# Kernel tuning notes

Measured on AMD Instinct MI355X. Metric: run time of the kernel, lower is better.

The kernel has to match this reference:

```python
import jax, jax.numpy as jnp
import numpy as np

H = 1024
S = 32768

def setup_inputs() -> dict:
    key = jax.random.key(0)
    k1, k2, k3, k4 = jax.random.split(key, 4)
    hidden = jax.random.normal(k1, (H,), dtype=jnp.float32)
    encoder_outputs = jax.random.normal(k2, (S, H), dtype=jnp.float32)
    # nn.Linear(H, H) params, scaled like torch default init
    bound = 1.0 / np.sqrt(H)
    W = jax.random.uniform(k3, (H, H), minval=-bound, maxval=bound, dtype=jnp.float32)
    b = jax.random.uniform(k4, (H,), minval=-bound, maxval=bound, dtype=jnp.float32)
    return {"hidden": hidden, "encoder_outputs": encoder_outputs, "W": W, "b": b}

def reference(hidden, encoder_outputs, W, b):
    # method == 'general': energy_i = hidden . (W @ e_i + b)
    # batched over all timesteps in one matmul instead of a Python loop
    proj = jnp.einsum('sh,dh->sd', encoder_outputs, W) + b  # [S, H]
    energies = proj @ hidden                                 # [S]
    attn = jax.nn.softmax(energies)                          # softmax over seq_len
    return attn[None, None, :]                               # [1, 1, S]
```

## Files before the change

### kernel.cpp

```cpp
#include <hip/hip_runtime.h>
#include <math.h>

#define H 1024
#define S 32768


__global__ __launch_bounds__(256) void compute_v(const float* __restrict__ W,
                                                 const float* __restrict__ hidden,
                                                 float* __restrict__ v) {
    int h = blockIdx.x * 256 + threadIdx.x;
    int d0 = blockIdx.y * 16;
    float acc = 0.f;
#pragma unroll
    for (int j = 0; j < 16; ++j) {
        int d = d0 + j;
        acc += W[(size_t)d * H + h] * hidden[d];
    }
    atomicAdd(&v[h], acc);
}

__global__ __launch_bounds__(256) void energies_kernel(const float* __restrict__ enc,
                                                       const float* __restrict__ v,
                                                       float* __restrict__ energies,
                                                       float* __restrict__ pmax,
                                                       float* __restrict__ psum) {
    const int lane = threadIdx.x & 63;
    const int wave = threadIdx.x >> 6;

    const float4* v4 = (const float4*)v;
    float4 va = v4[lane];
    float4 vb = v4[64 + lane];
    float4 vc = v4[128 + lane];
    float4 vd = v4[192 + lane];

    float m = -INFINITY;
    float sum = 0.f;

    int s0 = blockIdx.x * 32 + wave * 8;
#pragma unroll 1
    for (int r = 0; r < 8; ++r) {
        int s = s0 + r;
        const float4* row = (const float4*)(enc + (size_t)s * H);
        float4 a = row[lane];
        float4 b = row[64 + lane];
        float4 c = row[128 + lane];
        float4 d = row[192 + lane];
        float dot = a.x * va.x + a.y * va.y + a.z * va.z + a.w * va.w;
        dot += b.x * vb.x + b.y * vb.y + b.z * vb.z + b.w * vb.w;
        dot += c.x * vc.x + c.y * vc.y + c.z * vc.z + c.w * vc.w;
        dot += d.x * vd.x + d.y * vd.y + d.z * vd.z + d.w * vd.w;
#pragma unroll
        for (int off = 32; off > 0; off >>= 1) dot += __shfl_xor(dot, off, 64);
        if (lane == 0) energies[s] = dot;
        float mnew = fmaxf(m, dot);
        sum = sum * __expf(m - mnew) + __expf(dot - mnew);
        m = mnew;
    }

    __shared__ float wm[4], wsum[4];
    if (lane == 0) { wm[wave] = m; wsum[wave] = sum; }
    __syncthreads();
    if (threadIdx.x == 0) {
        float M = wm[0], Sm = wsum[0];
#pragma unroll
        for (int w = 1; w < 4; ++w) {
            float Mn = fmaxf(M, wm[w]);
            Sm = Sm * __expf(M - Mn) + wsum[w] * __expf(wm[w] - Mn);
            M = Mn;
        }
        pmax[blockIdx.x] = M;
        psum[blockIdx.x] = Sm;
    }
}

__global__ __launch_bounds__(1024) void combine(const float* __restrict__ pmax,
                                                const float* __restrict__ psum,
                                                float* __restrict__ MS) {
    int tid = threadIdx.x;
    float m = pmax[tid];
    float s = psum[tid];
    __shared__ float sm[1024];
    __shared__ float ss[1024];
    sm[tid] = m;
    __syncthreads();
    for (int off = 512; off > 0; off >>= 1) {
        if (tid < off) sm[tid] = fmaxf(sm[tid], sm[tid + off]);
        __syncthreads();
    }
    float M = sm[0];
    ss[tid] = s * __expf(m - M);
    __syncthreads();
    for (int off = 512; off > 0; off >>= 1) {
        if (tid < off) ss[tid] += ss[tid + off];
        __syncthreads();
    }
    if (tid == 0) {
        MS[0] = M;
        MS[1] = 1.0f / ss[0];
    }
}

__global__ __launch_bounds__(256) void finalize(float* __restrict__ out,
                                                const float* __restrict__ MS) {
    int i = blockIdx.x * 256 + threadIdx.x;
    float M = MS[0];
    float inv = MS[1];
    float4 e = ((const float4*)out)[i];
    float4 o;
    o.x = __expf(e.x - M) * inv;
    o.y = __expf(e.y - M) * inv;
    o.z = __expf(e.z - M) * inv;
    o.w = __expf(e.w - M) * inv;
    ((float4*)out)[i] = o;
}

extern "C" void kernel_launch(void* const* d_in, const int* in_sizes, int n_in,
                              void* d_out, int out_size, void* d_ws, size_t ws_size,
                              hipStream_t stream) {
    const float* hidden = (const float*)d_in[0];
    const float* enc    = (const float*)d_in[1];
    const float* W      = (const float*)d_in[2];

    float* ws   = (float*)d_ws;
    float* v    = ws;
    float* pmax = ws + 1024;
    float* psum = ws + 2048;
    float* MS   = ws + 3072;
    float* out  = (float*)d_out;

    hipMemsetAsync(v, 0, H * sizeof(float), stream);
    compute_v<<<dim3(4, 64), 256, 0, stream>>>(W, hidden, v);
    energies_kernel<<<S / 32, 256, 0, stream>>>(enc, v, out, pmax, psum);
    combine<<<1, 1024, 0, stream>>>(pmax, psum, MS);
    finalize<<<S / 4 / 256, 256, 0, stream>>>(out, MS);
}
```

Baseline: 205.9 us.

## Unroll energy rows per wave, double block count, shuffle-based combine

Each wave now handles 4 rows instead of 8. All 16 float4 loads for those rows are issued up front so more memory requests are in flight, and the four shuffle reductions are interleaved instead of running one per row. The grid doubles to 2048 blocks to give more parallelism on the bandwidth-bound pass over the 128MB encoder matrix. The combine kernel changes from a shared-memory tree with many barriers to wave shuffles plus one barrier, and it now merges 2048 partials. The workspace offsets are moved to fit the larger partial arrays.

```diff
diff --git a/kernel.cpp b/kernel.cpp
--- a/kernel.cpp
+++ b/kernel.cpp
@@ -33,29 +33,38 @@
     float4 vc = v4[128 + lane];
     float4 vd = v4[192 + lane];
 
-    float m = -INFINITY;
-    float sum = 0.f;
+    const int s0 = blockIdx.x * 16 + wave * 4;
+    const float4* base = (const float4*)(enc + (size_t)s0 * H);
 
-    int s0 = blockIdx.x * 32 + wave * 8;
-#pragma unroll 1
-    for (int r = 0; r < 8; ++r) {
-        int s = s0 + r;
-        const float4* row = (const float4*)(enc + (size_t)s * H);
+    float dot[4];
+#pragma unroll
+    for (int r = 0; r < 4; ++r) {
+        const float4* row = base + r * (H / 4);
         float4 a = row[lane];
         float4 b = row[64 + lane];
         float4 c = row[128 + lane];
         float4 d = row[192 + lane];
-        float dot = a.x * va.x + a.y * va.y + a.z * va.z + a.w * va.w;
-        dot += b.x * vb.x + b.y * vb.y + b.z * vb.z + b.w * vb.w;
-        dot += c.x * vc.x + c.y * vc.y + c.z * vc.z + c.w * vc.w;
-        dot += d.x * vd.x + d.y * vd.y + d.z * vd.z + d.w * vd.w;
+        float t = a.x * va.x + a.y * va.y + a.z * va.z + a.w * va.w;
+        t += b.x * vb.x + b.y * vb.y + b.z * vb.z + b.w * vb.w;
+        t += c.x * vc.x + c.y * vc.y + c.z * vc.z + c.w * vc.w;
+        t += d.x * vd.x + d.y * vd.y + d.z * vd.z + d.w * vd.w;
+        dot[r] = t;
+    }
+
 #pragma unroll
-        for (int off = 32; off > 0; off >>= 1) dot += __shfl_xor(dot, off, 64);
-        if (lane == 0) energies[s] = dot;
-        float mnew = fmaxf(m, dot);
-        sum = sum * __expf(m - mnew) + __expf(dot - mnew);
-        m = mnew;
+    for (int off = 32; off > 0; off >>= 1) {
+#pragma unroll
+        for (int r = 0; r < 4; ++r) dot[r] += __shfl_xor(dot[r], off, 64);
     }
+
+    if (lane == 0) {
+        float4 e = make_float4(dot[0], dot[1], dot[2], dot[3]);
+        *(float4*)(energies + s0) = e;
+    }
+
+    float m = fmaxf(fmaxf(dot[0], dot[1]), fmaxf(dot[2], dot[3]));
+    float sum = __expf(dot[0] - m) + __expf(dot[1] - m) +
+                __expf(dot[2] - m) + __expf(dot[3] - m);
 
     __shared__ float wm[4], wsum[4];
     if (lane == 0) { wm[wave] = m; wsum[wave] = sum; }
@@ -76,27 +85,42 @@
 __global__ __launch_bounds__(1024) void combine(const float* __restrict__ pmax,
                                                 const float* __restrict__ psum,
                                                 float* __restrict__ MS) {
-    int tid = threadIdx.x;
-    float m = pmax[tid];
-    float s = psum[tid];
-    __shared__ float sm[1024];
-    __shared__ float ss[1024];
-    sm[tid] = m;
+    const int tid = threadIdx.x;
+    const int lane = tid & 63;
+    const int wave = tid >> 6;
+
+    float m1 = pmax[tid], s1 = psum[tid];
+    float m2 = pmax[tid + 1024], s2 = psum[tid + 1024];
+    float M = fmaxf(m1, m2);
+    float Sv = s1 * __expf(m1 - M) + s2 * __expf(m2 - M);
+
+#pragma unroll
+    for (int off = 32; off > 0; off >>= 1) {
+        float Mo = __shfl_xor(M, off, 64);
+        float So = __shfl_xor(Sv, off, 64);
+        float Mn = fmaxf(M, Mo);
+        Sv = Sv * __expf(M - Mn) + So * __expf(Mo - Mn);
+        M = Mn;
+    }
+
+    __shared__ float sm[16], ss[16];
+    if (lane == 0) { sm[wave] = M; ss[wave] = Sv; }
     __syncthreads();
-    for (int off = 512; off > 0; off >>= 1) {
-        if (tid < off) sm[tid] = fmaxf(sm[tid], sm[tid + off]);
-        __syncthreads();
-    }
-    float M = sm[0];
-    ss[tid] = s * __expf(m - M);
-    __syncthreads();
-    for (int off = 512; off > 0; off >>= 1) {
-        if (tid < off) ss[tid] += ss[tid + off];
-        __syncthreads();
-    }
-    if (tid == 0) {
-        MS[0] = M;
-        MS[1] = 1.0f / ss[0];
+    if (wave == 0) {
+        float Mv = (lane < 16) ? sm[lane] : -INFINITY;
+        float Sw = (lane < 16) ? ss[lane] : 0.f;
+#pragma unroll
+        for (int off = 8; off > 0; off >>= 1) {
+            float Mo = __shfl_xor(Mv, off, 64);
+            float So = __shfl_xor(Sw, off, 64);
+            float Mn = fmaxf(Mv, Mo);
+            Sw = Sw * __expf(Mv - Mn) + So * __expf(Mo - Mn);
+            Mv = Mn;
+        }
+        if (lane == 0) {
+            MS[0] = Mv;
+            MS[1] = 1.0f / Sw;
+        }
     }
 }
 
@@ -124,13 +148,13 @@
     float* ws   = (float*)d_ws;
     float* v    = ws;
     float* pmax = ws + 1024;
-    float* psum = ws + 2048;
-    float* MS   = ws + 3072;
+    float* psum = ws + 3072;
+    float* MS   = ws + 5120;
     float* out  = (float*)d_out;
 
     hipMemsetAsync(v, 0, H * sizeof(float), stream);
     compute_v<<<dim3(4, 64), 256, 0, stream>>>(W, hidden, v);
-    energies_kernel<<<S / 32, 256, 0, stream>>>(enc, v, out, pmax, psum);
+    energies_kernel<<<S / 16, 256, 0, stream>>>(enc, v, out, pmax, psum);
     combine<<<1, 1024, 0, stream>>>(pmax, psum, MS);
     finalize<<<S / 4 / 256, 256, 0, stream>>>(out, MS);
 }
```

Result: no change. 203.5 us (-1.2%).
